# Performance work log

Hardware: AMD Instinct MI355X
Metric: run time of the kernel (lower is better)

Reference implementation:

```python
import jax, jax.numpy as jnp
import numpy as np

N_NODES = 100000
N_EDGES = 3200000
IN_FEAT = 128
HIDDEN = 32
NUM_LAYERS = 4
K = 35
NODES_PER_GRAPH = 100


def setup_inputs() -> dict:
    key = jax.random.key(0)
    ks = jax.random.split(key, 20)
    inp = {}
    inp['x'] = jax.random.normal(ks[0], (N_NODES, IN_FEAT), dtype=jnp.float32)
    inp['edge_index'] = jax.random.randint(ks[1], (2, N_EDGES), 0, N_NODES, dtype=jnp.int64)
    inp['batch'] = (jnp.arange(N_NODES, dtype=jnp.int64) // NODES_PER_GRAPH)
    # GCNConv weights (PyG: lin weight [in, out], bias [out])
    dims = [IN_FEAT] + [HIDDEN] * NUM_LAYERS
    for i in range(NUM_LAYERS):
        s = 1.0 / np.sqrt(dims[i])
        inp[f'w{i}'] = jax.random.normal(ks[2 + i], (dims[i], HIDDEN), dtype=jnp.float32) * s
        inp[f'b{i}'] = jnp.zeros((HIDDEN,), dtype=jnp.float32)
    # head: Conv1d(128->16,k=1), Conv1d(16->32,k=5), fc1(416->128), fc2(128->1)
    inp['conv1_w'] = jax.random.normal(ks[8], (16, HIDDEN * NUM_LAYERS, 1), dtype=jnp.float32) * (1.0 / np.sqrt(128))
    inp['conv1_b'] = jnp.zeros((16,), dtype=jnp.float32)
    inp['conv2_w'] = jax.random.normal(ks[9], (32, 16, 5), dtype=jnp.float32) * (1.0 / np.sqrt(16 * 5))
    inp['conv2_b'] = jnp.zeros((32,), dtype=jnp.float32)
    lin_in = 32 * (K // 2 - 4)  # 416
    inp['fc1_w'] = jax.random.normal(ks[10], (128, lin_in), dtype=jnp.float32) * (1.0 / np.sqrt(lin_in))
    inp['fc1_b'] = jnp.zeros((128,), dtype=jnp.float32)
    inp['fc2_w'] = jax.random.normal(ks[11], (1, 128), dtype=jnp.float32) * (1.0 / np.sqrt(128))
    inp['fc2_b'] = jnp.zeros((1,), dtype=jnp.float32)
    return inp


def _gcn_conv(x, w, b, src, dst, n):
    # PyG GCNConv: h = x @ W; add self-loops; sym-normalized scatter-add; + bias
    h = x @ w
    deg = jnp.ones((n,), h.dtype).at[dst].add(1.0)  # degree incl. self-loop
    dis = jax.lax.rsqrt(deg)
    coef = dis[src] * dis[dst]  # [E]
    agg = jax.ops.segment_sum(h[src] * coef[:, None], dst, num_segments=n)
    return agg + h / deg[:, None] + b  # self-loop norm = 1/deg


def reference(x, edge_index, batch, w0, b0, w1, b1, w2, b2, w3, b3,
              conv1_w, conv1_b, conv2_w, conv2_b, fc1_w, fc1_b, fc2_w, fc2_b):
    src, dst = edge_index[0], edge_index[1]
    n = x.shape[0]
    xs = []
    h = x
    for w, b in ((w0, b0), (w1, b1), (w2, b2), (w3, b3)):
        h = jnp.tanh(_gcn_conv(h, w, b, src, dst, n))
        xs.append(h)
    feat = jnp.concatenate(xs, axis=1)  # [N, 128]
    # global_sort_pool: graphs are contiguous blocks of NODES_PER_GRAPH nodes
    G = n // NODES_PER_GRAPH
    dense = feat.reshape(G, NODES_PER_GRAPH, -1)
    order = jnp.argsort(-dense[:, :, -1], axis=1)  # descending by last channel
    topk = jnp.take_along_axis(dense, order[:, :, None], axis=1)[:, :K]  # [G,K,128]
    y = topk.transpose(0, 2, 1)  # [G,128,K]
    y = jax.nn.relu(jnp.einsum('oc,gck->gok', conv1_w[:, :, 0], y) + conv1_b[None, :, None])
    L = y.shape[-1] // 2  # MaxPool1d(2), drop trailing element
    y = y[..., :L * 2].reshape(G, 16, L, 2).max(axis=-1)  # [G,16,17]
    y = jax.lax.conv_general_dilated(y, conv2_w, (1,), 'VALID',
                                     dimension_numbers=('NCH', 'OIH', 'NCH'))
    y = jax.nn.relu(y + conv2_b[None, :, None])  # [G,32,13]
    y = y.reshape(G, -1)  # [G,416]
    y = jax.nn.relu(y @ fc1_w.T + fc1_b)  # dropout is identity in eval
    return jax.nn.sigmoid(y @ fc2_w.T + fc2_b)  # [G,1]
```

## Files before the change

kernel.cpp:

```cpp
#include <hip/hip_runtime.h>
#include <hip/hip_fp16.h>
#include <math.h>

#define N_NODES 100000
#define N_EDGES 3200000
#define HIDDEN 32
#define K_TOP 35
#define NPG 100
#define N_GRAPHS 1000

#define BSHIFT 9
#define NLOC 512
#define NBUCK 196
#define CAP 17408
#define NBB 1024
#define BIN_CHUNK 13

typedef float vfloat4 __attribute__((ext_vector_type(4)));


__global__ void k_bin(const int* __restrict__ src, const int* __restrict__ dst,
                      int* __restrict__ bcnt, unsigned int* __restrict__ bdata) {
    __shared__ int h[NBUCK];
    __shared__ int lbase[NBUCK];
    __shared__ int lcur[NBUCK];
    int t = threadIdx.x;
    for (int i = t; i < NBUCK; i += 256) { h[i] = 0; lcur[i] = 0; }
    __syncthreads();
    int base = blockIdx.x * (256 * BIN_CHUNK);
    int ss[BIN_CHUNK], ds[BIN_CHUNK];
#pragma unroll
    for (int k = 0; k < BIN_CHUNK; k++) {
        int e = base + k * 256 + t;
        if (e < N_EDGES) {
            ss[k] = src[e];
            ds[k] = dst[e];
            atomicAdd(&h[ds[k] >> BSHIFT], 1);
        } else ds[k] = -1;
    }
    __syncthreads();
    for (int i = t; i < NBUCK; i += 256)
        lbase[i] = h[i] ? atomicAdd(&bcnt[i], h[i]) : 0;
    __syncthreads();
#pragma unroll
    for (int k = 0; k < BIN_CHUNK; k++) {
        int d = ds[k];
        if (d >= 0) {
            int bk = d >> BSHIFT;
            int pos = atomicAdd(&lcur[bk], 1);
            bdata[bk * CAP + lbase[bk] + pos] =
                ((unsigned int)ss[k] << BSHIFT) | (unsigned int)(d & (NLOC - 1));
        }
    }
}

__global__ void k_build(const unsigned int* __restrict__ bdata, const int* __restrict__ bcnt,
                        int* __restrict__ cnt, int* __restrict__ row_ptr,
                        float* __restrict__ dis, int* __restrict__ csr) {
    __shared__ int h[NLOC];
    __shared__ int sd[NLOC];
    __shared__ int rp[NLOC];
    __shared__ int cur[NLOC];
    int b = blockIdx.x, t = threadIdx.x;
    if (t < NLOC) h[t] = 0;
    __syncthreads();
    int r0 = b * CAP, r1 = r0 + bcnt[b];
    for (int i = r0 + t; i < r1; i += 1024)
        atomicAdd(&h[bdata[i] & (NLOC - 1)], 1);
    __syncthreads();
    int v = (t < NLOC) ? h[t] : 0;
    if (t < NLOC) sd[t] = v;
    __syncthreads();
    for (int off = 1; off < NLOC; off <<= 1) {
        int x = (t >= off && t < NLOC) ? sd[t - off] : 0;
        __syncthreads();
        if (t < NLOC) sd[t] += x;
        __syncthreads();
    }
    if (t < NLOC) {
        int excl = sd[t] - v;
        int node = (b << BSHIFT) + t;
        rp[t] = r0 + excl;
        cur[t] = 0;
        if (node < N_NODES) {
            cnt[node] = v;
            dis[node] = rsqrtf((float)(v + 1));
            row_ptr[node] = r0 + excl;
        }
    }
    __syncthreads();
    for (int i = r0 + t; i < r1; i += 1024) {
        unsigned int u = bdata[i];
        int loc = u & (NLOC - 1);
        int pos = atomicAdd(&cur[loc], 1);
        csr[rp[loc] + pos] = (int)(u >> BSHIFT);
    }
}


__global__ void k_mm0(const float* __restrict__ in, const float* __restrict__ w,
                      const float* __restrict__ dis, char* __restrict__ hs) {
    __shared__ float wl[128 * HIDDEN];
    int t = threadIdx.x;
    for (int i = t; i < 128 * HIDDEN; i += 256) wl[i] = w[i];
    __syncthreads();
    int n0 = blockIdx.x * 512 + t;
    int n1 = n0 + 256;
    bool has0 = n0 < N_NODES, has1 = n1 < N_NODES;
    int m0 = has0 ? n0 : 0, m1 = has1 ? n1 : 0;
    const float* r0p = in + (size_t)m0 * 128;
    const float* r1p = in + (size_t)m1 * 128;
    float acc0[HIDDEN], acc1[HIDDEN];
#pragma unroll
    for (int o = 0; o < HIDDEN; o++) { acc0[o] = 0.f; acc1[o] = 0.f; }
    for (int c4 = 0; c4 < 32; c4++) {
        float4 va = *(const float4*)(r0p + c4 * 4);
        float4 vb = *(const float4*)(r1p + c4 * 4);
        float xa[4] = {va.x, va.y, va.z, va.w};
        float xb[4] = {vb.x, vb.y, vb.z, vb.w};
#pragma unroll
        for (int k = 0; k < 4; k++) {
            const float* wr = &wl[(c4 * 4 + k) * HIDDEN];
#pragma unroll
            for (int o = 0; o < HIDDEN; o++) {
                float wv = wr[o];
                acc0[o] += xa[k] * wv;
                acc1[o] += xb[k] * wv;
            }
        }
    }
    if (has0) {
        float d = dis[m0];
        float4* hr = (float4*)(hs + (size_t)m0 * 64);
#pragma unroll
        for (int qq = 0; qq < 4; qq++) {
            __half2 p[4];
#pragma unroll
            for (int k = 0; k < 4; k++)
                p[k] = __floats2half2_rn(acc0[8 * qq + 2 * k] * d, acc0[8 * qq + 2 * k + 1] * d);
            hr[qq] = *(float4*)p;
        }
    }
    if (has1) {
        float d = dis[m1];
        float4* hr = (float4*)(hs + (size_t)m1 * 64);
#pragma unroll
        for (int qq = 0; qq < 4; qq++) {
            __half2 p[4];
#pragma unroll
            for (int k = 0; k < 4; k++)
                p[k] = __floats2half2_rn(acc1[8 * qq + 2 * k] * d, acc1[8 * qq + 2 * k + 1] * d);
            hr[qq] = *(float4*)p;
        }
    }
}

__global__ void k_agg(const float4* __restrict__ hs4, const float* __restrict__ dis,
                      const int* __restrict__ row_ptr, const int* __restrict__ cnt,
                      const int* __restrict__ csr_src, const float* __restrict__ bias,
                      float* __restrict__ feat, int col_off,
                      const float* __restrict__ wnext, char* __restrict__ hsn) {
    __shared__ float wl[32 * 33];
    __shared__ float tv[8][36];
    int tt = threadIdx.x;
    if (wnext) {
        for (int i = tt; i < 1024; i += 256)
            wl[(i >> 5) * 33 + (i & 31)] = wnext[i];
    }
    __syncthreads();
    int n = (blockIdx.x * 256 + tt) >> 5;
    int c = tt & 31;
    int r = c & 3;
    int ph = c >> 2;
    int slot = tt >> 5;
    int start = row_ptr[n];
    int m = cnt[n];
    float d = dis[n];
    float aA[8] = {0, 0, 0, 0, 0, 0, 0, 0};
    float aB[8] = {0, 0, 0, 0, 0, 0, 0, 0};

    for (int base = 0; base < m; base += 32) {
        int e = base + c;
        int idx = (e < m) ? csr_src[start + e] : 0;
        int id0 = __shfl(idx, ph, 32);
        int id1 = __shfl(idx, 8 + ph, 32);
        int id2 = __shfl(idx, 16 + ph, 32);
        int id3 = __shfl(idx, 24 + ph, 32);
        bool v0 = base + ph < m;
        bool v1 = base + 8 + ph < m;
        bool v2 = base + 16 + ph < m;
        bool v3 = base + 24 + ph < m;
        float4 g0 = hs4[(size_t)(v0 ? id0 : n) * 4 + r];
        float4 g1 = hs4[(size_t)(v1 ? id1 : n) * 4 + r];
        float4 g2 = hs4[(size_t)(v2 ? id2 : n) * 4 + r];
        float4 g3 = hs4[(size_t)(v3 ? id3 : n) * 4 + r];
        const __half2* h0 = (const __half2*)&g0;
        const __half2* h1 = (const __half2*)&g1;
        const __half2* h2 = (const __half2*)&g2;
        const __half2* h3 = (const __half2*)&g3;
        float2 f;
        if (v0) {
            f = __half22float2(h0[0]); aA[0] += f.x; aA[1] += f.y;
            f = __half22float2(h0[1]); aA[2] += f.x; aA[3] += f.y;
            f = __half22float2(h0[2]); aA[4] += f.x; aA[5] += f.y;
            f = __half22float2(h0[3]); aA[6] += f.x; aA[7] += f.y;
        }
        if (v1) {
            f = __half22float2(h1[0]); aB[0] += f.x; aB[1] += f.y;
            f = __half22float2(h1[1]); aB[2] += f.x; aB[3] += f.y;
            f = __half22float2(h1[2]); aB[4] += f.x; aB[5] += f.y;
            f = __half22float2(h1[3]); aB[6] += f.x; aB[7] += f.y;
        }
        if (v2) {
            f = __half22float2(h2[0]); aA[0] += f.x; aA[1] += f.y;
            f = __half22float2(h2[1]); aA[2] += f.x; aA[3] += f.y;
            f = __half22float2(h2[2]); aA[4] += f.x; aA[5] += f.y;
            f = __half22float2(h2[3]); aA[6] += f.x; aA[7] += f.y;
        }
        if (v3) {
            f = __half22float2(h3[0]); aB[0] += f.x; aB[1] += f.y;
            f = __half22float2(h3[1]); aB[2] += f.x; aB[3] += f.y;
            f = __half22float2(h3[2]); aB[4] += f.x; aB[5] += f.y;
            f = __half22float2(h3[3]); aB[6] += f.x; aB[7] += f.y;
        }
    }
    float s[8];
#pragma unroll
    for (int k = 0; k < 8; k++) {
        float v = aA[k] + aB[k];
        v += __shfl_xor(v, 4);
        v += __shfl_xor(v, 8);
        v += __shfl_xor(v, 16);
        s[k] = v;
    }
    float s01 = (ph & 1) ? s[1] : s[0];
    float s23 = (ph & 1) ? s[3] : s[2];
    float s45 = (ph & 1) ? s[5] : s[4];
    float s67 = (ph & 1) ? s[7] : s[6];
    float s03 = (ph & 2) ? s23 : s01;
    float s47 = (ph & 2) ? s67 : s45;
    float sp  = (ph & 4) ? s47 : s03;
    float4 sv = hs4[(size_t)n * 4 + r];
    const __half2* sh = (const __half2*)&sv;
    __half2 q01 = (ph & 2) ? sh[1] : sh[0];
    __half2 q23 = (ph & 2) ? sh[3] : sh[2];
    __half2 qq  = (ph & 4) ? q23 : q01;
    float self = (ph & 1) ? __high2float(qq) : __low2float(qq);
    float bv = bias[8 * r + ph];
    float ov = tanhf(d * (sp + self) + bv);
    __builtin_nontemporal_store(ov, &feat[(size_t)n * 128 + col_off + 8 * r + ph]);
    if (wnext) {
        tv[slot][8 * r + ph] = ov;
        __builtin_amdgcn_wave_barrier();
        float o = 0.f;
#pragma unroll 8
        for (int k = 0; k < 32; k++)
            o += tv[slot][k] * wl[k * 33 + c];
        o *= d;
        float oh = __shfl_xor(o, 1);
        if ((c & 1) == 0) {
            __half2 pck = __floats2half2_rn(o, oh);
            *(__half2*)(hsn + (size_t)n * 64 + (size_t)c * 2) = pck;
        }
    }
}


__global__ void __launch_bounds__(256, 4)
k_head(const float* __restrict__ feat,
       const float* __restrict__ c1w, const float* __restrict__ c1b,
       const float* __restrict__ c2w, const float* __restrict__ c2b,
       const float* __restrict__ f1w, const float* __restrict__ f1b,
       const float* __restrict__ f2w, const float* __restrict__ f2b,
       float* __restrict__ out) {
    __shared__ float vals[NPG];
    __shared__ int sel[K_TOP];
    __shared__ float tk[K_TOP * 132];
    __shared__ float wl1[16 * 129];
    __shared__ float y1[16][36];
    __shared__ float y2[16][17];
    __shared__ float y3[416];
    __shared__ float y4[128];
    __shared__ float r2[128];
    int g = blockIdx.x, t = threadIdx.x;
    const float* fg = feat + (size_t)g * NPG * 128;

    for (int i = t; i < 2048; i += 256)
        wl1[(i >> 7) * 129 + (i & 127)] = c1w[i];
    if (t < NPG) vals[t] = fg[t * 128 + 127];
    __syncthreads();
    if (t < NPG) {
        float v = vals[t];
        int r = 0;
        for (int j = 0; j < NPG; j++) {
            float u = vals[j];
            r += (u > v) || (u == v && j < t);
        }
        if (r < K_TOP) sel[r] = t;
    }
    __syncthreads();
    for (int i = t; i < K_TOP * 32; i += 256) {
        int k = i >> 5, c4 = i & 31;
        *(float4*)&tk[k * 132 + 4 * c4] = *(const float4*)&fg[sel[k] * 128 + 4 * c4];
    }
    __syncthreads();
    for (int i = t; i < 16 * K_TOP; i += 256) {
        int o = i & 15, k = i >> 4;
        float s = c1b[o];
        const float* wr = &wl1[o * 129];
        const float* xr = &tk[k * 132];
#pragma unroll 8
        for (int c = 0; c < 128; c++) s += wr[c] * xr[c];
        y1[o][k] = fmaxf(s, 0.f);
    }
    __syncthreads();
    for (int i = t; i < 16 * 17; i += 256) {
        int o = i & 15, l = i >> 4;
        y2[o][l] = fmaxf(y1[o][2 * l], y1[o][2 * l + 1]);
    }
    __syncthreads();
    for (int idx = t; idx < 32 * 13; idx += 256) {
        int o2 = idx / 13, ttp = idx - o2 * 13;
        float s = c2b[o2];
        const float* wr = c2w + o2 * 80;
#pragma unroll
        for (int i = 0; i < 16; i++)
#pragma unroll
            for (int j = 0; j < 5; j++) s += wr[i * 5 + j] * y2[i][ttp + j];
        y3[idx] = fmaxf(s, 0.f);
    }
    __syncthreads();
    {
        int o = t >> 1, h = t & 1;
        const float4* wr4 = (const float4*)(f1w + o * 416) + h * 52;
        const float* yb = y3 + h * 208;
        float s = 0.f;
#pragma unroll 4
        for (int i = 0; i < 52; i++) {
            float4 w4 = wr4[i];
            s += w4.x * yb[4 * i] + w4.y * yb[4 * i + 1] +
                 w4.z * yb[4 * i + 2] + w4.w * yb[4 * i + 3];
        }
        s += __shfl_xor(s, 1);
        if (h == 0) y4[o] = fmaxf(s + f1b[o], 0.f);
    }
    __syncthreads();
    if (t < 128) r2[t] = f2w[t] * y4[t];
    __syncthreads();
    for (int off = 64; off > 0; off >>= 1) {
        if (t < off) r2[t] += r2[t + off];
        __syncthreads();
    }
    if (t == 0) out[g] = 1.0f / (1.0f + expf(-(r2[0] + f2b[0])));
}


static inline size_t alignup(size_t x) { return (x + 255) & ~(size_t)255; }

extern "C" void kernel_launch(void* const* d_in, const int* in_sizes, int n_in,
                              void* d_out, int out_size, void* d_ws, size_t ws_size,
                              hipStream_t stream) {
    const float* x    = (const float*)d_in[0];
    const int*   ei   = (const int*)d_in[1];
    const int*   srcp = ei;
    const int*   dstp = ei + N_EDGES;
    const float* w0 = (const float*)d_in[3];
    const float* b0 = (const float*)d_in[4];
    const float* w1 = (const float*)d_in[5];
    const float* b1 = (const float*)d_in[6];
    const float* w2 = (const float*)d_in[7];
    const float* b2 = (const float*)d_in[8];
    const float* w3 = (const float*)d_in[9];
    const float* b3 = (const float*)d_in[10];
    const float* c1w = (const float*)d_in[11];
    const float* c1b = (const float*)d_in[12];
    const float* c2w = (const float*)d_in[13];
    const float* c2b = (const float*)d_in[14];
    const float* f1w = (const float*)d_in[15];
    const float* f1b = (const float*)d_in[16];
    const float* f2w = (const float*)d_in[17];
    const float* f2b = (const float*)d_in[18];
    float* out = (float*)d_out;

    char* p = (char*)d_ws;
    int* cnt     = (int*)p; p += alignup(sizeof(int) * N_NODES);
    int* row_ptr = (int*)p; p += alignup(sizeof(int) * N_NODES);
    float* dis   = (float*)p; p += alignup(sizeof(float) * N_NODES);
    int* bcnt    = (int*)p; p += alignup(sizeof(int) * NBUCK);
    int* csr     = (int*)p; p += alignup(sizeof(int) * (size_t)NBUCK * CAP);
    char* U = p;
    unsigned int* bdata = (unsigned int*)U;
    char* hsA = U;
    char* hsB = U + alignup((size_t)N_NODES * 64);
    size_t usz = alignup(sizeof(unsigned int) * (size_t)NBUCK * CAP);
    float* feat = (float*)(U + usz);

    const int NB_M = (N_NODES + 511) / 512;
    const int NB_A = (N_NODES * 32) / 256;

    hipMemsetAsync(bcnt, 0, sizeof(int) * NBUCK, stream);
    k_bin<<<NBB, 256, 0, stream>>>(srcp, dstp, bcnt, bdata);
    k_build<<<NBUCK, 1024, 0, stream>>>(bdata, bcnt, cnt, row_ptr, dis, csr);

    k_mm0<<<NB_M, 256, 0, stream>>>(x, w0, dis, hsA);
    k_agg<<<NB_A, 256, 0, stream>>>((const float4*)hsA, dis, row_ptr, cnt, csr, b0,
                                    feat, 0, w1, hsB);
    k_agg<<<NB_A, 256, 0, stream>>>((const float4*)hsB, dis, row_ptr, cnt, csr, b1,
                                    feat, 32, w2, hsA);
    k_agg<<<NB_A, 256, 0, stream>>>((const float4*)hsA, dis, row_ptr, cnt, csr, b2,
                                    feat, 64, w3, hsB);
    k_agg<<<NB_A, 256, 0, stream>>>((const float4*)hsB, dis, row_ptr, cnt, csr, b3,
                                    feat, 96, (const float*)nullptr, (char*)nullptr);

    k_head<<<N_GRAPHS, 256, 0, stream>>>(feat, c1w, c1b, c2w, c2b,
                                         f1w, f1b, f2w, f2b, out);
}
```

Baseline: 413.9 us.

## Accumulate neighbor sums in half2, pad zero sentinel row, split mm0 rows

The aggregation kernel now accumulates gathered neighbor features with packed half2 adds instead of converting each value to fp32. Out-of-range edge slots point at a zeroed sentinel row (index N_NODES) instead of using per-lane validity predicates, which removes branching from the gather loop. The first matmul kernel now splits each node's 128 input channels across two threads and combines the halves with a shuffle, doubling parallelism and halving registers per thread. Accumulating in fp16 risks precision loss and overflow on high-degree nodes, and the sentinel rows need extra memsets.

```diff
diff --git a/kernel.cpp b/kernel.cpp
--- a/kernel.cpp
+++ b/kernel.cpp
@@ -15,8 +15,6 @@
 #define CAP 17408
 #define NBB 1024
 #define BIN_CHUNK 13
-
-typedef float vfloat4 __attribute__((ext_vector_type(4)));
 
 
 __global__ void k_bin(const int* __restrict__ src, const int* __restrict__ dst,
@@ -104,53 +102,45 @@
     int t = threadIdx.x;
     for (int i = t; i < 128 * HIDDEN; i += 256) wl[i] = w[i];
     __syncthreads();
-    int n0 = blockIdx.x * 512 + t;
-    int n1 = n0 + 256;
-    bool has0 = n0 < N_NODES, has1 = n1 < N_NODES;
-    int m0 = has0 ? n0 : 0, m1 = has1 ? n1 : 0;
-    const float* r0p = in + (size_t)m0 * 128;
-    const float* r1p = in + (size_t)m1 * 128;
-    float acc0[HIDDEN], acc1[HIDDEN];
-#pragma unroll
-    for (int o = 0; o < HIDDEN; o++) { acc0[o] = 0.f; acc1[o] = 0.f; }
-    for (int c4 = 0; c4 < 32; c4++) {
-        float4 va = *(const float4*)(r0p + c4 * 4);
-        float4 vb = *(const float4*)(r1p + c4 * 4);
+    int gt = blockIdx.x * 256 + t;
+    int n = gt >> 1, hh = gt & 1;
+    if (n >= N_NODES) return;
+    const float* rp = in + (size_t)n * 128 + hh * 64;
+    const float* wbase = &wl[hh * 64 * HIDDEN];
+    float acc[HIDDEN];
+#pragma unroll
+    for (int o = 0; o < HIDDEN; o++) acc[o] = 0.f;
+    for (int c4 = 0; c4 < 16; c4++) {
+        float4 va = *(const float4*)(rp + c4 * 4);
         float xa[4] = {va.x, va.y, va.z, va.w};
-        float xb[4] = {vb.x, vb.y, vb.z, vb.w};
 #pragma unroll
         for (int k = 0; k < 4; k++) {
-            const float* wr = &wl[(c4 * 4 + k) * HIDDEN];
-#pragma unroll
-            for (int o = 0; o < HIDDEN; o++) {
-                float wv = wr[o];
-                acc0[o] += xa[k] * wv;
-                acc1[o] += xb[k] * wv;
-            }
-        }
-    }
-    if (has0) {
-        float d = dis[m0];
-        float4* hr = (float4*)(hs + (size_t)m0 * 64);
-#pragma unroll
-        for (int qq = 0; qq < 4; qq++) {
+            const float* wr = &wbase[(c4 * 4 + k) * HIDDEN];
+#pragma unroll
+            for (int o = 0; o < HIDDEN; o++) acc[o] += xa[k] * wr[o];
+        }
+    }
+#pragma unroll
+    for (int o = 0; o < HIDDEN; o++) acc[o] += __shfl_xor(acc[o], 1);
+    float d = dis[n];
+    float4* hr = (float4*)(hs + (size_t)n * 64);
+    if (hh == 0) {
+#pragma unroll
+        for (int q = 0; q < 2; q++) {
             __half2 p[4];
 #pragma unroll
-            for (int k = 0; k < 4; k++)
-                p[k] = __floats2half2_rn(acc0[8 * qq + 2 * k] * d, acc0[8 * qq + 2 * k + 1] * d);
-            hr[qq] = *(float4*)p;
-        }
-    }
-    if (has1) {
-        float d = dis[m1];
-        float4* hr = (float4*)(hs + (size_t)m1 * 64);
-#pragma unroll
-        for (int qq = 0; qq < 4; qq++) {
+            for (int kk = 0; kk < 4; kk++)
+                p[kk] = __floats2half2_rn(acc[8 * q + 2 * kk] * d, acc[8 * q + 2 * kk + 1] * d);
+            hr[q] = *(float4*)p;
+        }
+    } else {
+#pragma unroll
+        for (int q = 0; q < 2; q++) {
             __half2 p[4];
 #pragma unroll
-            for (int k = 0; k < 4; k++)
-                p[k] = __floats2half2_rn(acc1[8 * qq + 2 * k] * d, acc1[8 * qq + 2 * k + 1] * d);
-            hr[qq] = *(float4*)p;
+            for (int kk = 0; kk < 4; kk++)
+                p[kk] = __floats2half2_rn(acc[16 + 8 * q + 2 * kk] * d, acc[16 + 8 * q + 2 * kk + 1] * d);
+            hr[2 + q] = *(float4*)p;
         }
     }
 }
@@ -176,62 +166,44 @@
     int start = row_ptr[n];
     int m = cnt[n];
     float d = dis[n];
-    float aA[8] = {0, 0, 0, 0, 0, 0, 0, 0};
-    float aB[8] = {0, 0, 0, 0, 0, 0, 0, 0};
+    __half2 z = __floats2half2_rn(0.f, 0.f);
+    __half2 a0[4], a1[4], a2[4], a3[4];
+#pragma unroll
+    for (int j = 0; j < 4; j++) { a0[j] = z; a1[j] = z; a2[j] = z; a3[j] = z; }
 
     for (int base = 0; base < m; base += 32) {
         int e = base + c;
-        int idx = (e < m) ? csr_src[start + e] : 0;
+        int idx = (e < m) ? csr_src[start + e] : N_NODES;
         int id0 = __shfl(idx, ph, 32);
         int id1 = __shfl(idx, 8 + ph, 32);
         int id2 = __shfl(idx, 16 + ph, 32);
         int id3 = __shfl(idx, 24 + ph, 32);
-        bool v0 = base + ph < m;
-        bool v1 = base + 8 + ph < m;
-        bool v2 = base + 16 + ph < m;
-        bool v3 = base + 24 + ph < m;
-        float4 g0 = hs4[(size_t)(v0 ? id0 : n) * 4 + r];
-        float4 g1 = hs4[(size_t)(v1 ? id1 : n) * 4 + r];
-        float4 g2 = hs4[(size_t)(v2 ? id2 : n) * 4 + r];
-        float4 g3 = hs4[(size_t)(v3 ? id3 : n) * 4 + r];
+        float4 g0 = hs4[(size_t)id0 * 4 + r];
+        float4 g1 = hs4[(size_t)id1 * 4 + r];
+        float4 g2 = hs4[(size_t)id2 * 4 + r];
+        float4 g3 = hs4[(size_t)id3 * 4 + r];
         const __half2* h0 = (const __half2*)&g0;
         const __half2* h1 = (const __half2*)&g1;
         const __half2* h2 = (const __half2*)&g2;
         const __half2* h3 = (const __half2*)&g3;
-        float2 f;
-        if (v0) {
-            f = __half22float2(h0[0]); aA[0] += f.x; aA[1] += f.y;
-            f = __half22float2(h0[1]); aA[2] += f.x; aA[3] += f.y;
-            f = __half22float2(h0[2]); aA[4] += f.x; aA[5] += f.y;
-            f = __half22float2(h0[3]); aA[6] += f.x; aA[7] += f.y;
-        }
-        if (v1) {
-            f = __half22float2(h1[0]); aB[0] += f.x; aB[1] += f.y;
-            f = __half22float2(h1[1]); aB[2] += f.x; aB[3] += f.y;
-            f = __half22float2(h1[2]); aB[4] += f.x; aB[5] += f.y;
-            f = __half22float2(h1[3]); aB[6] += f.x; aB[7] += f.y;
-        }
-        if (v2) {
-            f = __half22float2(h2[0]); aA[0] += f.x; aA[1] += f.y;
-            f = __half22float2(h2[1]); aA[2] += f.x; aA[3] += f.y;
-            f = __half22float2(h2[2]); aA[4] += f.x; aA[5] += f.y;
-            f = __half22float2(h2[3]); aA[6] += f.x; aA[7] += f.y;
-        }
-        if (v3) {
-            f = __half22float2(h3[0]); aB[0] += f.x; aB[1] += f.y;
-            f = __half22float2(h3[1]); aB[2] += f.x; aB[3] += f.y;
-            f = __half22float2(h3[2]); aB[4] += f.x; aB[5] += f.y;
-            f = __half22float2(h3[3]); aB[6] += f.x; aB[7] += f.y;
+#pragma unroll
+        for (int j = 0; j < 4; j++) {
+            a0[j] = __hadd2(a0[j], h0[j]);
+            a1[j] = __hadd2(a1[j], h1[j]);
+            a2[j] = __hadd2(a2[j], h2[j]);
+            a3[j] = __hadd2(a3[j], h3[j]);
         }
     }
     float s[8];
 #pragma unroll
-    for (int k = 0; k < 8; k++) {
-        float v = aA[k] + aB[k];
-        v += __shfl_xor(v, 4);
-        v += __shfl_xor(v, 8);
-        v += __shfl_xor(v, 16);
-        s[k] = v;
+    for (int j = 0; j < 4; j++) {
+        __half2 m2 = __hadd2(__hadd2(a0[j], a1[j]), __hadd2(a2[j], a3[j]));
+        float2 f = __half22float2(m2);
+        float v0 = f.x, v1 = f.y;
+        v0 += __shfl_xor(v0, 4); v0 += __shfl_xor(v0, 8); v0 += __shfl_xor(v0, 16);
+        v1 += __shfl_xor(v1, 4); v1 += __shfl_xor(v1, 8); v1 += __shfl_xor(v1, 16);
+        s[2 * j] = v0;
+        s[2 * j + 1] = v1;
     }
     float s01 = (ph & 1) ? s[1] : s[0];
     float s23 = (ph & 1) ? s[3] : s[2];
@@ -391,16 +363,19 @@
     char* U = p;
     unsigned int* bdata = (unsigned int*)U;
     char* hsA = U;
-    char* hsB = U + alignup((size_t)N_NODES * 64);
+    char* hsB = U + alignup((size_t)N_NODES * 64 + 64);
     size_t usz = alignup(sizeof(unsigned int) * (size_t)NBUCK * CAP);
     float* feat = (float*)(U + usz);
 
-    const int NB_M = (N_NODES + 511) / 512;
+    const int NB_M = (N_NODES * 2 + 255) / 256;
     const int NB_A = (N_NODES * 32) / 256;
 
     hipMemsetAsync(bcnt, 0, sizeof(int) * NBUCK, stream);
     k_bin<<<NBB, 256, 0, stream>>>(srcp, dstp, bcnt, bdata);
     k_build<<<NBUCK, 1024, 0, stream>>>(bdata, bcnt, cnt, row_ptr, dis, csr);
+
+    hipMemsetAsync(hsA + (size_t)N_NODES * 64, 0, 64, stream);
+    hipMemsetAsync(hsB + (size_t)N_NODES * 64, 0, 64, stream);
 
     k_mm0<<<NB_M, 256, 0, stream>>>(x, w0, dis, hsA);
     k_agg<<<NB_A, 256, 0, stream>>>((const float4*)hsA, dis, row_ptr, cnt, csr, b0,
```

New measurement: 425.0 us. 1.03x slower.

## Use a full 64-lane wave per node in aggregation with zero-padded sentinel row

Applied to the files above, without the earlier changes.

The aggregation kernel now assigns one 64-lane wavefront per node instead of 32 lanes, gathering 16 edges per iteration and adding one extra cross-lane reduction step. Out-of-range edges now point to a zero-filled sentinel row appended to each feature buffer, which removes the per-edge validity branches. Row pointer and count are packed into one int2 array so both come from a single load. The change doubles the number of launched threads and splits the next-layer matmul across both half-waves, so low-degree nodes may waste more lanes.

```diff
diff --git a/kernel.cpp b/kernel.cpp
--- a/kernel.cpp
+++ b/kernel.cpp
@@ -15,8 +15,6 @@
 #define CAP 17408
 #define NBB 1024
 #define BIN_CHUNK 13
-
-typedef float vfloat4 __attribute__((ext_vector_type(4)));
 
 
 __global__ void k_bin(const int* __restrict__ src, const int* __restrict__ dst,
@@ -55,8 +53,8 @@
 }
 
 __global__ void k_build(const unsigned int* __restrict__ bdata, const int* __restrict__ bcnt,
-                        int* __restrict__ cnt, int* __restrict__ row_ptr,
-                        float* __restrict__ dis, int* __restrict__ csr) {
+                        int2* __restrict__ rc, float* __restrict__ dis,
+                        int* __restrict__ csr) {
     __shared__ int h[NLOC];
     __shared__ int sd[NLOC];
     __shared__ int rp[NLOC];
@@ -83,9 +81,8 @@
         rp[t] = r0 + excl;
         cur[t] = 0;
         if (node < N_NODES) {
-            cnt[node] = v;
+            rc[node] = make_int2(r0 + excl, v);
             dis[node] = rsqrtf((float)(v + 1));
-            row_ptr[node] = r0 + excl;
         }
     }
     __syncthreads();
@@ -156,111 +153,104 @@
 }
 
 __global__ void k_agg(const float4* __restrict__ hs4, const float* __restrict__ dis,
-                      const int* __restrict__ row_ptr, const int* __restrict__ cnt,
-                      const int* __restrict__ csr_src, const float* __restrict__ bias,
+                      const int2* __restrict__ rc, const int* __restrict__ csr_src,
+                      const float* __restrict__ bias,
                       float* __restrict__ feat, int col_off,
                       const float* __restrict__ wnext, char* __restrict__ hsn) {
     __shared__ float wl[32 * 33];
-    __shared__ float tv[8][36];
+    __shared__ float tv[4][36];
     int tt = threadIdx.x;
     if (wnext) {
         for (int i = tt; i < 1024; i += 256)
             wl[(i >> 5) * 33 + (i & 31)] = wnext[i];
     }
     __syncthreads();
-    int n = (blockIdx.x * 256 + tt) >> 5;
-    int c = tt & 31;
+    int n = (blockIdx.x * 256 + tt) >> 6;
+    int c = tt & 63;
     int r = c & 3;
     int ph = c >> 2;
-    int slot = tt >> 5;
-    int start = row_ptr[n];
-    int m = cnt[n];
+    int p7 = ph & 7;
+    int slot = tt >> 6;
+    int2 rcv = rc[n];
+    int start = rcv.x, m = rcv.y;
     float d = dis[n];
-    float aA[8] = {0, 0, 0, 0, 0, 0, 0, 0};
-    float aB[8] = {0, 0, 0, 0, 0, 0, 0, 0};
-
-    for (int base = 0; base < m; base += 32) {
+    float4 sv = hs4[(size_t)n * 4 + r];
+    float acc[8] = {0.f, 0.f, 0.f, 0.f, 0.f, 0.f, 0.f, 0.f};
+
+    for (int base = 0; base < m; base += 64) {
         int e = base + c;
-        int idx = (e < m) ? csr_src[start + e] : 0;
-        int id0 = __shfl(idx, ph, 32);
-        int id1 = __shfl(idx, 8 + ph, 32);
-        int id2 = __shfl(idx, 16 + ph, 32);
-        int id3 = __shfl(idx, 24 + ph, 32);
-        bool v0 = base + ph < m;
-        bool v1 = base + 8 + ph < m;
-        bool v2 = base + 16 + ph < m;
-        bool v3 = base + 24 + ph < m;
-        float4 g0 = hs4[(size_t)(v0 ? id0 : n) * 4 + r];
-        float4 g1 = hs4[(size_t)(v1 ? id1 : n) * 4 + r];
-        float4 g2 = hs4[(size_t)(v2 ? id2 : n) * 4 + r];
-        float4 g3 = hs4[(size_t)(v3 ? id3 : n) * 4 + r];
+        int idx = (e < m) ? csr_src[start + e] : N_NODES;
+        int id0 = __shfl(idx, ph, 64);
+        int id1 = __shfl(idx, 16 + ph, 64);
+        int id2 = __shfl(idx, 32 + ph, 64);
+        int id3 = __shfl(idx, 48 + ph, 64);
+        float4 g0 = hs4[(size_t)id0 * 4 + r];
+        float4 g1 = hs4[(size_t)id1 * 4 + r];
+        float4 g2 = hs4[(size_t)id2 * 4 + r];
+        float4 g3 = hs4[(size_t)id3 * 4 + r];
         const __half2* h0 = (const __half2*)&g0;
         const __half2* h1 = (const __half2*)&g1;
         const __half2* h2 = (const __half2*)&g2;
         const __half2* h3 = (const __half2*)&g3;
         float2 f;
-        if (v0) {
-            f = __half22float2(h0[0]); aA[0] += f.x; aA[1] += f.y;
-            f = __half22float2(h0[1]); aA[2] += f.x; aA[3] += f.y;
-            f = __half22float2(h0[2]); aA[4] += f.x; aA[5] += f.y;
-            f = __half22float2(h0[3]); aA[6] += f.x; aA[7] += f.y;
-        }
-        if (v1) {
-            f = __half22float2(h1[0]); aB[0] += f.x; aB[1] += f.y;
-            f = __half22float2(h1[1]); aB[2] += f.x; aB[3] += f.y;
-            f = __half22float2(h1[2]); aB[4] += f.x; aB[5] += f.y;
-            f = __half22float2(h1[3]); aB[6] += f.x; aB[7] += f.y;
-        }
-        if (v2) {
-            f = __half22float2(h2[0]); aA[0] += f.x; aA[1] += f.y;
-            f = __half22float2(h2[1]); aA[2] += f.x; aA[3] += f.y;
-            f = __half22float2(h2[2]); aA[4] += f.x; aA[5] += f.y;
-            f = __half22float2(h2[3]); aA[6] += f.x; aA[7] += f.y;
-        }
-        if (v3) {
-            f = __half22float2(h3[0]); aB[0] += f.x; aB[1] += f.y;
-            f = __half22float2(h3[1]); aB[2] += f.x; aB[3] += f.y;
-            f = __half22float2(h3[2]); aB[4] += f.x; aB[5] += f.y;
-            f = __half22float2(h3[3]); aB[6] += f.x; aB[7] += f.y;
+#pragma unroll
+        for (int j = 0; j < 4; j++) {
+            f = __half22float2(h0[j]); acc[2 * j] += f.x; acc[2 * j + 1] += f.y;
+        }
+#pragma unroll
+        for (int j = 0; j < 4; j++) {
+            f = __half22float2(h1[j]); acc[2 * j] += f.x; acc[2 * j + 1] += f.y;
+        }
+#pragma unroll
+        for (int j = 0; j < 4; j++) {
+            f = __half22float2(h2[j]); acc[2 * j] += f.x; acc[2 * j + 1] += f.y;
+        }
+#pragma unroll
+        for (int j = 0; j < 4; j++) {
+            f = __half22float2(h3[j]); acc[2 * j] += f.x; acc[2 * j + 1] += f.y;
         }
     }
     float s[8];
 #pragma unroll
     for (int k = 0; k < 8; k++) {
-        float v = aA[k] + aB[k];
+        float v = acc[k];
         v += __shfl_xor(v, 4);
         v += __shfl_xor(v, 8);
         v += __shfl_xor(v, 16);
+        v += __shfl_xor(v, 32);
         s[k] = v;
     }
-    float s01 = (ph & 1) ? s[1] : s[0];
-    float s23 = (ph & 1) ? s[3] : s[2];
-    float s45 = (ph & 1) ? s[5] : s[4];
-    float s67 = (ph & 1) ? s[7] : s[6];
-    float s03 = (ph & 2) ? s23 : s01;
-    float s47 = (ph & 2) ? s67 : s45;
-    float sp  = (ph & 4) ? s47 : s03;
-    float4 sv = hs4[(size_t)n * 4 + r];
+    float s01 = (p7 & 1) ? s[1] : s[0];
+    float s23 = (p7 & 1) ? s[3] : s[2];
+    float s45 = (p7 & 1) ? s[5] : s[4];
+    float s67 = (p7 & 1) ? s[7] : s[6];
+    float s03 = (p7 & 2) ? s23 : s01;
+    float s47 = (p7 & 2) ? s67 : s45;
+    float sp  = (p7 & 4) ? s47 : s03;
     const __half2* sh = (const __half2*)&sv;
-    __half2 q01 = (ph & 2) ? sh[1] : sh[0];
-    __half2 q23 = (ph & 2) ? sh[3] : sh[2];
-    __half2 qq  = (ph & 4) ? q23 : q01;
-    float self = (ph & 1) ? __high2float(qq) : __low2float(qq);
-    float bv = bias[8 * r + ph];
+    __half2 q01 = (p7 & 2) ? sh[1] : sh[0];
+    __half2 q23 = (p7 & 2) ? sh[3] : sh[2];
+    __half2 qq  = (p7 & 4) ? q23 : q01;
+    float self = (p7 & 1) ? __high2float(qq) : __low2float(qq);
+    float bv = bias[8 * r + p7];
     float ov = tanhf(d * (sp + self) + bv);
-    __builtin_nontemporal_store(ov, &feat[(size_t)n * 128 + col_off + 8 * r + ph]);
+    if (ph < 8)
+        __builtin_nontemporal_store(ov, &feat[(size_t)n * 128 + col_off + 8 * r + p7]);
     if (wnext) {
-        tv[slot][8 * r + ph] = ov;
+        if (ph < 8) tv[slot][8 * r + p7] = ov;
         __builtin_amdgcn_wave_barrier();
+        int cc = c & 31;
+        int kbase = (c >> 5) * 16;
         float o = 0.f;
 #pragma unroll 8
-        for (int k = 0; k < 32; k++)
-            o += tv[slot][k] * wl[k * 33 + c];
+        for (int k2 = 0; k2 < 16; k2++)
+            o += tv[slot][kbase + k2] * wl[(kbase + k2) * 33 + cc];
+        o += __shfl_xor(o, 32);
         o *= d;
         float oh = __shfl_xor(o, 1);
-        if ((c & 1) == 0) {
+        if (c < 32 && (c & 1) == 0) {
             __half2 pck = __floats2half2_rn(o, oh);
-            *(__half2*)(hsn + (size_t)n * 64 + (size_t)c * 2) = pck;
+            *(__half2*)(hsn + (size_t)n * 64 + (size_t)cc * 2) = pck;
         }
     }
 }
@@ -383,33 +373,35 @@
     float* out = (float*)d_out;
 
     char* p = (char*)d_ws;
-    int* cnt     = (int*)p; p += alignup(sizeof(int) * N_NODES);
-    int* row_ptr = (int*)p; p += alignup(sizeof(int) * N_NODES);
+    int2* rcv    = (int2*)p; p += alignup(sizeof(int2) * N_NODES);
     float* dis   = (float*)p; p += alignup(sizeof(float) * N_NODES);
     int* bcnt    = (int*)p; p += alignup(sizeof(int) * NBUCK);
     int* csr     = (int*)p; p += alignup(sizeof(int) * (size_t)NBUCK * CAP);
     char* U = p;
     unsigned int* bdata = (unsigned int*)U;
     char* hsA = U;
-    char* hsB = U + alignup((size_t)N_NODES * 64);
+    char* hsB = U + alignup((size_t)N_NODES * 64 + 64);
     size_t usz = alignup(sizeof(unsigned int) * (size_t)NBUCK * CAP);
     float* feat = (float*)(U + usz);
 
     const int NB_M = (N_NODES + 511) / 512;
-    const int NB_A = (N_NODES * 32) / 256;
+    const int NB_A = (N_NODES * 64) / 256;
 
     hipMemsetAsync(bcnt, 0, sizeof(int) * NBUCK, stream);
     k_bin<<<NBB, 256, 0, stream>>>(srcp, dstp, bcnt, bdata);
-    k_build<<<NBUCK, 1024, 0, stream>>>(bdata, bcnt, cnt, row_ptr, dis, csr);
+    k_build<<<NBUCK, 1024, 0, stream>>>(bdata, bcnt, rcv, dis, csr);
+
+    hipMemsetAsync(hsA + (size_t)N_NODES * 64, 0, 64, stream);
+    hipMemsetAsync(hsB + (size_t)N_NODES * 64, 0, 64, stream);
 
     k_mm0<<<NB_M, 256, 0, stream>>>(x, w0, dis, hsA);
-    k_agg<<<NB_A, 256, 0, stream>>>((const float4*)hsA, dis, row_ptr, cnt, csr, b0,
+    k_agg<<<NB_A, 256, 0, stream>>>((const float4*)hsA, dis, rcv, csr, b0,
                                     feat, 0, w1, hsB);
-    k_agg<<<NB_A, 256, 0, stream>>>((const float4*)hsB, dis, row_ptr, cnt, csr, b1,
+    k_agg<<<NB_A, 256, 0, stream>>>((const float4*)hsB, dis, rcv, csr, b1,
                                     feat, 32, w2, hsA);
-    k_agg<<<NB_A, 256, 0, stream>>>((const float4*)hsA, dis, row_ptr, cnt, csr, b2,
+    k_agg<<<NB_A, 256, 0, stream>>>((const float4*)hsA, dis, rcv, csr, b2,
                                     feat, 64, w3, hsB);
-    k_agg<<<NB_A, 256, 0, stream>>>((const float4*)hsB, dis, row_ptr, cnt, csr, b3,
+    k_agg<<<NB_A, 256, 0, stream>>>((const float4*)hsB, dis, rcv, csr, b3,
                                     feat, 96, (const float*)nullptr, (char*)nullptr);
 
     k_head<<<N_GRAPHS, 256, 0, stream>>>(feat, c1w, c1b, c2w, c2b,
```

Result: slower. 480.9 us (+16.2%).
